# Optimization experiments

Hardware: AMD Instinct MI355X
Metric: run time of the kernel (lower is better)

## Reference

```python
import jax, jax.numpy as jnp
import numpy as np

NUM_AA = 21  # amino-acid alphabet size


def setup_inputs() -> dict:
    key = jax.random.key(0)
    k_x, k_q, k_k, k_v = jax.random.split(key, 4)
    B, L, H, D = 64, 512, 32, 128
    x = jax.random.randint(k_x, (B, L), 0, NUM_AA, dtype=jnp.int32)
    Q = jax.random.normal(k_q, (H, L, D), dtype=jnp.float32)
    K = jax.random.normal(k_k, (H, L, D), dtype=jnp.float32)
    V = jax.random.normal(k_v, (H, NUM_AA, NUM_AA), dtype=jnp.float32)
    return {"x": x, "Q": Q, "K": K, "V": V}


def reference(x, Q, K, V):
    # x: [B, L] int indices in [0, 21); Q,K: [H, L, d_k]; V: [H, q, q]
    d_k = Q.shape[-1]
    L = Q.shape[1]
    # attention over positions, per head: [H, L, L]
    scores = jnp.einsum('hid,hjd->hij', Q, K) / d_k
    A = jax.nn.softmax(scores, axis=-1)
    # coupling tensor J[i, j, a, b] = sum_h A[h, i, j] * V[h, a, b]  -> [L, L, q, q]
    J = jnp.einsum('hij,hab->ijab', A, V)
    # energy[b] = -sum_{i,j} J[i, j, x[b,i], x[b,j]]
    ii = jnp.arange(L)[:, None]        # [L, 1]
    jj = jnp.arange(L)[None, :]        # [1, L]
    vals = J[ii, jj, x[:, :, None], x[:, None, :]]  # broadcast gather -> [B, L, L]
    energy = -jnp.sum(vals, axis=(1, 2))            # [B]
    return energy
```

## Files before the change

### kernel.cpp

```cpp
#include <hip/hip_runtime.h>
#include <hip/hip_bf16.h>
#include <stdint.h>

#define NH  32
#define NL  512
#define ND  128
#define NB  64
#define NAA 21

#define EW_OFF 0
#define QB_OFF (16u << 20)
#define KB_OFF (18u << 20)
#define ZG_OFF (20u << 20)

typedef short bf16x8 __attribute__((ext_vector_type(8)));
typedef float f32x4  __attribute__((ext_vector_type(4)));

static __device__ __forceinline__ uint32_t bf16rtn(float f) {
    uint32_t u = __float_as_uint(f);
    return (u + 0x7fffu + ((u >> 16) & 1u)) >> 16;
}
static __device__ __forceinline__ void gl16(const void* g, void* l) {
    __builtin_amdgcn_global_load_lds(
        (const __attribute__((address_space(1))) uint32_t*)g,
        (__attribute__((address_space(3))) uint32_t*)l, 16, 0, 0);
}

__global__ void prep_qk(const float* __restrict__ Q, const float* __restrict__ K,
                        uint32_t* __restrict__ Qb, uint32_t* __restrict__ Kb) {
    uint32_t tid = blockIdx.x * 256 + threadIdx.x;
    const float* src = (tid >> 20) ? K : Q;
    uint32_t*    dst = (tid >> 20) ? Kb : Qb;
    uint32_t p = tid & 0xFFFFFu;
    uint32_t kk2 = p & 31, r = (p >> 5) & 63, dc = (p >> 11) & 1;
    uint32_t pt = (p >> 12) & 7, h = p >> 15;
    uint32_t pos = pt * 64 + r, d0 = dc * 64 + kk2 * 2;
    float2 v = *(const float2*)(src + ((size_t)(h * NL + pos) * ND + d0));
    uint32_t val = bf16rtn(v.x) | (bf16rtn(v.y) << 16);
    uint32_t byte = (r * 128 + kk2 * 4) ^ ((r & 7) << 4);
    dst[((((h * 8 + pt) * 2 + dc)) << 11) + (byte >> 2)] = val;
}

#define SC_QS 0
#define SC_KS 16384
#define SC_ZS 49152
#define SC_TOT 49408

__global__ __launch_bounds__(512)
void scores_mfma(const uint8_t* __restrict__ Qb, const uint8_t* __restrict__ Kb,
                 uint8_t* __restrict__ Ewsw, float* __restrict__ Zg) {
    extern __shared__ uint8_t smem[];
    int h = blockIdx.x >> 3, it = blockIdx.x & 7;
    int t = threadIdx.x, lane = t & 63, wv = t >> 6;
    int wm = wv >> 1, wn = wv & 1;

    const uint8_t* qsrc = Qb + (((size_t)(h * 8 + it) * 2) << 13);
    gl16(qsrc + t * 16,        smem + SC_QS + t * 16);
    gl16(qsrc + 8192 + t * 16, smem + SC_QS + 8192 + t * 16);
    if (t < 64) *(float*)(smem + SC_ZS + t * 4) = 0.f;

    float zp[2] = {0.f, 0.f};
    for (int sc = 0; sc < 4; ++sc) {
        __syncthreads();
        const uint8_t* ksrc = Kb + (((size_t)(h * 8 + sc * 2) * 2) << 13);
#pragma unroll
        for (int q = 0; q < 4; ++q)
            gl16(ksrc + q * 8192 + t * 16, smem + SC_KS + q * 8192 + t * 16);
        __syncthreads();

        f32x4 acc[2][2];
#pragma unroll
        for (int fm = 0; fm < 2; ++fm)
#pragma unroll
            for (int fn = 0; fn < 2; ++fn) acc[fm][fn] = (f32x4){0.f,0.f,0.f,0.f};

#pragma unroll
        for (int ks = 0; ks < 4; ++ks) {
            int kb = ((ks & 1) * 32 + (lane >> 4) * 8) * 2;
            int dc = ks >> 1;
            bf16x8 af[2], bfr[2];
#pragma unroll
            for (int fm = 0; fm < 2; ++fm) {
                int rr = wm * 32 + fm * 16 + (lane & 15);
                int rt = rr >> 6, r6 = rr & 63;
                af[fm] = *(bf16x8*)(smem + SC_KS + (rt * 2 + dc) * 8192 +
                          (((uint32_t)(r6 * 128 + kb)) ^ ((r6 & 7) << 4)));
            }
#pragma unroll
            for (int fn = 0; fn < 2; ++fn) {
                int rr = wn * 32 + fn * 16 + (lane & 15);
                bfr[fn] = *(bf16x8*)(smem + SC_QS + dc * 8192 +
                          (((uint32_t)(rr * 128 + kb)) ^ ((rr & 7) << 4)));
            }
#pragma unroll
            for (int fm = 0; fm < 2; ++fm)
#pragma unroll
                for (int fn = 0; fn < 2; ++fn)
                    acc[fm][fn] = __builtin_amdgcn_mfma_f32_16x16x32_bf16(
                        af[fm], bfr[fn], acc[fm][fn], 0, 0, 0);
        }
#pragma unroll
        for (int fm = 0; fm < 2; ++fm)
#pragma unroll
            for (int fn = 0; fn < 2; ++fn) {
                float e0 = __expf(acc[fm][fn][0] * 0.0078125f);
                float e1 = __expf(acc[fm][fn][1] * 0.0078125f);
                float e2 = __expf(acc[fm][fn][2] * 0.0078125f);
                float e3 = __expf(acc[fm][fn][3] * 0.0078125f);
                zp[fn] += (e0 + e1) + (e2 + e3);
                uint2 pk;
                pk.x = bf16rtn(e0) | (bf16rtn(e1) << 16);
                pk.y = bf16rtn(e2) | (bf16rtn(e3) << 16);
                int j = sc * 128 + wm * 32 + fm * 16 + (lane >> 4) * 4;
                int i = wn * 32 + fn * 16 + (lane & 15);
                int kc = j >> 6, kk = j & 63;
                uint32_t byte = ((uint32_t)(i * 128 + kk * 2)) ^ ((uint32_t)((i & 7) << 4));
                *(uint2*)(Ewsw + (((size_t)((h * 8 + it) * 8 + kc)) << 13) + byte) = pk;
            }
    }
    zp[0] += __shfl_xor(zp[0], 16); zp[0] += __shfl_xor(zp[0], 32);
    zp[1] += __shfl_xor(zp[1], 16); zp[1] += __shfl_xor(zp[1], 32);
    if (lane < 16) {
        atomicAdd((float*)(smem + SC_ZS) + wn * 32 + lane,      zp[0]);
        atomicAdd((float*)(smem + SC_ZS) + wn * 32 + 16 + lane, zp[1]);
    }
    __syncthreads();
    if (t < 64) Zg[(size_t)h * NL + it * 64 + t] = *((float*)(smem + SC_ZS) + t);
}

#define GE_AB   0
#define GE_RACC 0
#define GE_XS   32768
#define GE_VS   38016
#define GE_TOT  39808

__global__ __launch_bounds__(512, 4)
void gemm_energy(const uint8_t* __restrict__ Ew, const int* __restrict__ x,
                 const float* __restrict__ Zg, const float* __restrict__ V,
                 float* __restrict__ out) {
    extern __shared__ uint8_t smem[];
    uint32_t* xs = (uint32_t*)(smem + GE_XS);
    float*    Vs = (float*)(smem + GE_VS);
    float*    Racc = (float*)(smem + GE_RACC);

    int bid = blockIdx.x;
    int xcd = bid & 7, q = bid >> 3;
    int nb = q % 7, g = (q / 7) * 8 + xcd;
    int h = g >> 2, it = g & 3;
    int n0 = nb * 192;
    int bstart = n0 / 21;
    int bend = (n0 + 191) / 21;
    int bcnt = bend - bstart + 1;

    int t = threadIdx.x, lane = t & 63, wv = t >> 6;
    int wm = wv >> 2, wn = wv & 3;

    const uint8_t* A0 = Ew + (((size_t)(h * 8 + it * 2) * 8) << 13);
    const uint8_t* A1 = Ew + (((size_t)(h * 8 + it * 2 + 1) * 8) << 13);
#define GE_STAGE(p, kc) do { \
        gl16(A0 + (((size_t)(kc)) << 13) + t * 16, smem + GE_AB + (p) * 16384 + t * 16); \
        gl16(A1 + (((size_t)(kc)) << 13) + t * 16, smem + GE_AB + (p) * 16384 + 8192 + t * 16); \
    } while (0)
    GE_STAGE(0, 0);

    for (int idx = t; idx < bcnt * 128; idx += 512) {
        int s = idx >> 7, w = idx & 127;
        int4 xv = *(const int4*)(x + (size_t)(bstart + s) * NL + w * 4);
        xs[s * 129 + w] = (uint32_t)(xv.x & 0xff) | ((uint32_t)(xv.y & 0xff) << 8)
                        | ((uint32_t)(xv.z & 0xff) << 16) | ((uint32_t)(xv.w & 0xff) << 24);
    }
    for (int idx = t; idx < NAA * NAA; idx += 512) Vs[idx] = V[h * (NAA * NAA) + idx];

    int ccol[3], slotc[3];
#pragma unroll
    for (int fn = 0; fn < 3; ++fn) {
        int n = n0 + wn * 48 + fn * 16 + (lane & 15);
        int b = n / 21;
        ccol[fn] = n - b * 21;
        slotc[fn] = b - bstart;
    }

    f32x4 acc[4][3];
#pragma unroll
    for (int fm = 0; fm < 4; ++fm)
#pragma unroll
        for (int fn = 0; fn < 3; ++fn) acc[fm][fn] = (f32x4){0.f,0.f,0.f,0.f};

    __syncthreads();

    for (int kc = 0; kc < 8; ++kc) {
        int p = kc & 1;
        if (kc < 7) GE_STAGE(p ^ 1, kc + 1);
#pragma unroll
        for (int ks = 0; ks < 2; ++ks) {
            int kb = (ks * 32 + (lane >> 4) * 8) * 2;
            bf16x8 af[4];
#pragma unroll
            for (int fm = 0; fm < 4; ++fm) {
                int r6 = fm * 16 + (lane & 15);
                af[fm] = *(bf16x8*)(smem + GE_AB + p * 16384 + wm * 8192 +
                          (((uint32_t)(r6 * 128 + kb)) ^ ((r6 & 7) << 4)));
            }
            int k0w = kc * 16 + ks * 8 + (lane >> 4) * 2;
            bf16x8 bfr[3];
#pragma unroll
            for (int fn = 0; fn < 3; ++fn) {
                uint32_t w0 = xs[slotc[fn] * 129 + k0w];
                uint32_t w1 = xs[slotc[fn] * 129 + k0w + 1];
                uint32_t c = (uint32_t)ccol[fn];
                union { uint32_t u[4]; bf16x8 v; } pk;
#pragma unroll
                for (int pq = 0; pq < 4; ++pq) {
                    uint32_t w = (pq < 2) ? w0 : w1;
                    uint32_t sh = (pq & 1) * 16;
                    uint32_t b0 = (w >> sh) & 0xffu, b1 = (w >> (sh + 8)) & 0xffu;
                    pk.u[pq] = ((b0 == c) ? 0x3F80u : 0u) | ((b1 == c) ? 0x3F800000u : 0u);
                }
                bfr[fn] = pk.v;
            }
#pragma unroll
            for (int fm = 0; fm < 4; ++fm)
#pragma unroll
                for (int fn = 0; fn < 3; ++fn)
                    acc[fm][fn] = __builtin_amdgcn_mfma_f32_16x16x32_bf16(
                        af[fm], bfr[fn], acc[fm][fn], 0, 0, 0);
        }
        __syncthreads();
    }

    float vsum = 0.f;
    int srow = lane & 31;
    int s = wv * 2 + (lane >> 5);
#pragma unroll
    for (int w = 0; w < 4; ++w) {
        if (wm == (w >> 1)) {
#pragma unroll
            for (int f = 0; f < 2; ++f) {
                int fm = (w & 1) * 2 + f;
#pragma unroll
                for (int fn = 0; fn < 3; ++fn) {
                    int col = wn * 48 + fn * 16 + (lane & 15);
                    int rb = f * 16 + (lane >> 4) * 4;
#pragma unroll
                    for (int r = 0; r < 4; ++r)
                        Racc[(rb + r) * 193 + col] = acc[fm][fn][r];
                }
            }
        }
        __syncthreads();
        int ig = it * 128 + w * 32 + srow;
        float rz = 1.0f / Zg[(size_t)h * NL + ig];
        if (s < bcnt) {
            int b = bstart + s;
            uint32_t xw = xs[s * 129 + (ig >> 2)];
            int a = (int)((xw >> ((ig & 3) * 8)) & 0xffu);
            int off = b * 21 - n0;
            int clo = off < 0 ? -off : 0;
            int chi = (192 - off) < 21 ? (192 - off) : 21;
            float dot = 0.f;
            for (int c = clo; c < chi; ++c)
                dot += Vs[a * NAA + c] * Racc[srow * 193 + off + c];
            vsum += dot * rz;
        }
        __syncthreads();
    }
#pragma unroll
    for (int o = 1; o < 32; o <<= 1) vsum += __shfl_xor(vsum, o);
    if (srow == 0 && s < bcnt) atomicAdd(&out[bstart + s], -vsum);
}

extern "C" void kernel_launch(void* const* d_in, const int* in_sizes, int n_in,
                              void* d_out, int out_size, void* d_ws, size_t ws_size,
                              hipStream_t stream) {
    const int*   x = (const int*)d_in[0];
    const float* Q = (const float*)d_in[1];
    const float* K = (const float*)d_in[2];
    const float* V = (const float*)d_in[3];
    float* out = (float*)d_out;
    uint8_t* ws = (uint8_t*)d_ws;

    uint8_t*  Ewsw = ws + EW_OFF;
    uint32_t* Qb   = (uint32_t*)(ws + QB_OFF);
    uint32_t* Kb   = (uint32_t*)(ws + KB_OFF);
    float*    Zg   = (float*)(ws + ZG_OFF);

    hipMemsetAsync(d_out, 0, NB * sizeof(float), stream);
    prep_qk<<<8192, 256, 0, stream>>>(Q, K, Qb, Kb);
    (void)hipFuncSetAttribute((const void*)scores_mfma,
                              hipFuncAttributeMaxDynamicSharedMemorySize, SC_TOT);
    scores_mfma<<<256, 512, SC_TOT, stream>>>((const uint8_t*)Qb, (const uint8_t*)Kb,
                                              Ewsw, Zg);
    (void)hipFuncSetAttribute((const void*)gemm_energy,
                              hipFuncAttributeMaxDynamicSharedMemorySize, GE_TOT);
    gemm_energy<<<896, 512, GE_TOT, stream>>>((const uint8_t*)Ewsw, x, Zg, V, out);
}
```

Before: 79.34 us.

## Precompute one-hot B fragments in a separate kernel and load them from global

Adds a prep kernel that builds the bf16 one-hot B-operand MFMA fragments from x once and writes them to workspace in fragment order. The energy GEMM then loads those fragments from global/L2 instead of rebuilding them per block from LDS with compares and shifts. It also hoists the swizzled A-fragment LDS offsets out of the loop. The trade is an extra kernel launch plus global traffic for B fragments, which are reread by many blocks, in exchange for less ALU and LDS work in the inner loop.

```diff
diff --git a/kernel.cpp b/kernel.cpp
--- a/kernel.cpp
+++ b/kernel.cpp
@@ -12,6 +12,7 @@
 #define QB_OFF (16u << 20)
 #define KB_OFF (18u << 20)
 #define ZG_OFF (20u << 20)
+#define BF_OFF (21u << 20)
 
 typedef short bf16x8 __attribute__((ext_vector_type(8)));
 typedef float f32x4  __attribute__((ext_vector_type(4)));
@@ -39,6 +40,30 @@
     uint32_t val = bf16rtn(v.x) | (bf16rtn(v.y) << 16);
     uint32_t byte = (r * 128 + kk2 * 4) ^ ((r & 7) << 4);
     dst[((((h * 8 + pt) * 2 + dc)) << 11) + (byte >> 2)] = val;
+}
+
+__global__ void prep_bfrag(const int* __restrict__ x, uint8_t* __restrict__ Bf) {
+    int tid = blockIdx.x * 256 + threadIdx.x;
+    int lane = tid & 63;
+    int f  = tid >> 6;
+    int cg = f % 12;
+    int t2 = f / 12;
+    int ks = t2 & 1;
+    int t3 = t2 >> 1;
+    int kc = t3 & 7;
+    int nb = t3 >> 3;
+    int col = nb * 192 + cg * 16 + (lane & 15);
+    int b = col / 21, c = col - b * 21;
+    int k0 = kc * 64 + ks * 32 + (lane >> 4) * 8;
+    const int* xp = x + (size_t)b * NL + k0;
+    int4 x0 = *(const int4*)(xp);
+    int4 x1 = *(const int4*)(xp + 4);
+    uint4 pk;
+    pk.x = ((x0.x == c) ? 0x3F80u : 0u) | ((x0.y == c) ? 0x3F800000u : 0u);
+    pk.y = ((x0.z == c) ? 0x3F80u : 0u) | ((x0.w == c) ? 0x3F800000u : 0u);
+    pk.z = ((x1.x == c) ? 0x3F80u : 0u) | ((x1.y == c) ? 0x3F800000u : 0u);
+    pk.w = ((x1.z == c) ? 0x3F80u : 0u) | ((x1.w == c) ? 0x3F800000u : 0u);
+    *(uint4*)(Bf + (size_t)tid * 16) = pk;
 }
 
 #define SC_QS 0
@@ -135,9 +160,9 @@
 #define GE_TOT  39808
 
 __global__ __launch_bounds__(512, 4)
-void gemm_energy(const uint8_t* __restrict__ Ew, const int* __restrict__ x,
-                 const float* __restrict__ Zg, const float* __restrict__ V,
-                 float* __restrict__ out) {
+void gemm_energy(const uint8_t* __restrict__ Ew, const uint8_t* __restrict__ Bf,
+                 const int* __restrict__ x, const float* __restrict__ Zg,
+                 const float* __restrict__ V, float* __restrict__ out) {
     extern __shared__ uint8_t smem[];
     uint32_t* xs = (uint32_t*)(smem + GE_XS);
     float*    Vs = (float*)(smem + GE_VS);
@@ -171,14 +196,18 @@
     }
     for (int idx = t; idx < NAA * NAA; idx += 512) Vs[idx] = V[h * (NAA * NAA) + idx];
 
-    int ccol[3], slotc[3];
-#pragma unroll
-    for (int fn = 0; fn < 3; ++fn) {
-        int n = n0 + wn * 48 + fn * 16 + (lane & 15);
-        int b = n / 21;
-        ccol[fn] = n - b * 21;
-        slotc[fn] = b - bstart;
-    }
+    const uint8_t* bfw = Bf + ((size_t)(nb * 192 + 3 * wn)) * 1024 + lane * 16;
+
+    uint32_t aoff[2][4];
+#pragma unroll
+    for (int ks = 0; ks < 2; ++ks)
+#pragma unroll
+        for (int fm = 0; fm < 4; ++fm) {
+            int r6 = fm * 16 + (lane & 15);
+            int kb = (ks * 32 + (lane >> 4) * 8) * 2;
+            aoff[ks][fm] = (uint32_t)(wm * 8192 +
+                           (((uint32_t)(r6 * 128 + kb)) ^ ((r6 & 7) << 4)));
+        }
 
     f32x4 acc[4][3];
 #pragma unroll
@@ -191,39 +220,24 @@
     for (int kc = 0; kc < 8; ++kc) {
         int p = kc & 1;
         if (kc < 7) GE_STAGE(p ^ 1, kc + 1);
+        bf16x8 bfr[2][3];
+#pragma unroll
+        for (int ks = 0; ks < 2; ++ks)
+#pragma unroll
+            for (int fn = 0; fn < 3; ++fn)
+                bfr[ks][fn] = *(const bf16x8*)(bfw + kc * 24576 + ks * 12288 + fn * 1024);
 #pragma unroll
         for (int ks = 0; ks < 2; ++ks) {
-            int kb = (ks * 32 + (lane >> 4) * 8) * 2;
             bf16x8 af[4];
 #pragma unroll
-            for (int fm = 0; fm < 4; ++fm) {
-                int r6 = fm * 16 + (lane & 15);
-                af[fm] = *(bf16x8*)(smem + GE_AB + p * 16384 + wm * 8192 +
-                          (((uint32_t)(r6 * 128 + kb)) ^ ((r6 & 7) << 4)));
-            }
-            int k0w = kc * 16 + ks * 8 + (lane >> 4) * 2;
-            bf16x8 bfr[3];
-#pragma unroll
-            for (int fn = 0; fn < 3; ++fn) {
-                uint32_t w0 = xs[slotc[fn] * 129 + k0w];
-                uint32_t w1 = xs[slotc[fn] * 129 + k0w + 1];
-                uint32_t c = (uint32_t)ccol[fn];
-                union { uint32_t u[4]; bf16x8 v; } pk;
-#pragma unroll
-                for (int pq = 0; pq < 4; ++pq) {
-                    uint32_t w = (pq < 2) ? w0 : w1;
-                    uint32_t sh = (pq & 1) * 16;
-                    uint32_t b0 = (w >> sh) & 0xffu, b1 = (w >> (sh + 8)) & 0xffu;
-                    pk.u[pq] = ((b0 == c) ? 0x3F80u : 0u) | ((b1 == c) ? 0x3F800000u : 0u);
-                }
-                bfr[fn] = pk.v;
-            }
+            for (int fm = 0; fm < 4; ++fm)
+                af[fm] = *(bf16x8*)(smem + GE_AB + p * 16384 + aoff[ks][fm]);
 #pragma unroll
             for (int fm = 0; fm < 4; ++fm)
 #pragma unroll
                 for (int fn = 0; fn < 3; ++fn)
                     acc[fm][fn] = __builtin_amdgcn_mfma_f32_16x16x32_bf16(
-                        af[fm], bfr[fn], acc[fm][fn], 0, 0, 0);
+                        af[fm], bfr[ks][fn], acc[fm][fn], 0, 0, 0);
         }
         __syncthreads();
     }
@@ -283,14 +297,16 @@
     uint32_t* Qb   = (uint32_t*)(ws + QB_OFF);
     uint32_t* Kb   = (uint32_t*)(ws + KB_OFF);
     float*    Zg   = (float*)(ws + ZG_OFF);
+    uint8_t*  Bfr  = ws + BF_OFF;
 
     hipMemsetAsync(d_out, 0, NB * sizeof(float), stream);
     prep_qk<<<8192, 256, 0, stream>>>(Q, K, Qb, Kb);
+    prep_bfrag<<<336, 256, 0, stream>>>(x, Bfr);
     (void)hipFuncSetAttribute((const void*)scores_mfma,
                               hipFuncAttributeMaxDynamicSharedMemorySize, SC_TOT);
     scores_mfma<<<256, 512, SC_TOT, stream>>>((const uint8_t*)Qb, (const uint8_t*)Kb,
                                               Ewsw, Zg);
     (void)hipFuncSetAttribute((const void*)gemm_energy,
                               hipFuncAttributeMaxDynamicSharedMemorySize, GE_TOT);
-    gemm_energy<<<896, 512, GE_TOT, stream>>>((const uint8_t*)Ewsw, x, Zg, V, out);
-}
+    gemm_energy<<<896, 512, GE_TOT, stream>>>((const uint8_t*)Ewsw, Bfr, x, Zg, V, out);
+}
```

After: 78.73 us. About the same (-0.8%).

## Fuse scores and energy GEMM into one kernel keeping exp-scores in LDS

Applied to the files above, without the earlier changes.

Merges the scores kernel and the energy GEMM kernel into a single kernel. Each block computes its 64-row tile of exponentiated scores into LDS, then runs the one-hot GEMM over all 64 batches (21 accumulator fragments per wave) and the V contraction directly from LDS. This removes the global round trip of the score matrix and the row-sum array, plus one launch. In exchange the kernel uses about 150KB of LDS with only 256 blocks, and the wide accumulator array raises register pressure and lowers occupancy.

```diff
diff --git a/kernel.cpp b/kernel.cpp
--- a/kernel.cpp
+++ b/kernel.cpp
@@ -8,10 +8,8 @@
 #define NB  64
 #define NAA 21
 
-#define EW_OFF 0
 #define QB_OFF (16u << 20)
 #define KB_OFF (18u << 20)
-#define ZG_OFF (20u << 20)
 
 typedef short bf16x8 __attribute__((ext_vector_type(8)));
 typedef float f32x4  __attribute__((ext_vector_type(4)));
@@ -41,232 +39,182 @@
     dst[((((h * 8 + pt) * 2 + dc)) << 11) + (byte >> 2)] = val;
 }
 
-#define SC_QS 0
-#define SC_KS 16384
-#define SC_ZS 49152
-#define SC_TOT 49408
-
-__global__ __launch_bounds__(512)
-void scores_mfma(const uint8_t* __restrict__ Qb, const uint8_t* __restrict__ Kb,
-                 uint8_t* __restrict__ Ewsw, float* __restrict__ Zg) {
+#define FA_A   0
+#define FA_STG 65536
+#define FA_XS  114688
+#define FA_VS  147968
+#define FA_ZS  149760
+#define FA_TOT 150016
+
+__global__ __launch_bounds__(512, 2)
+void fused_energy(const uint8_t* __restrict__ Qb, const uint8_t* __restrict__ Kb,
+                  const int* __restrict__ x, const float* __restrict__ V,
+                  float* __restrict__ out) {
     extern __shared__ uint8_t smem[];
+    uint8_t*  Al  = smem + FA_A;
+    uint32_t* xs  = (uint32_t*)(smem + FA_XS);
+    float*    Vs  = (float*)(smem + FA_VS);
+    float*    Zl  = (float*)(smem + FA_ZS);
+    float*    Racc = (float*)(smem + FA_STG);
+
     int h = blockIdx.x >> 3, it = blockIdx.x & 7;
     int t = threadIdx.x, lane = t & 63, wv = t >> 6;
-    int wm = wv >> 1, wn = wv & 1;
 
     const uint8_t* qsrc = Qb + (((size_t)(h * 8 + it) * 2) << 13);
-    gl16(qsrc + t * 16,        smem + SC_QS + t * 16);
-    gl16(qsrc + 8192 + t * 16, smem + SC_QS + 8192 + t * 16);
-    if (t < 64) *(float*)(smem + SC_ZS + t * 4) = 0.f;
-
-    float zp[2] = {0.f, 0.f};
-    for (int sc = 0; sc < 4; ++sc) {
+    gl16(qsrc + t * 16,        smem + FA_STG + t * 16);
+    gl16(qsrc + 8192 + t * 16, smem + FA_STG + 8192 + t * 16);
+    for (int idx = t; idx < 64 * 128; idx += 512) {
+        int s = idx >> 7, w = idx & 127;
+        int4 xv = *(const int4*)(x + (size_t)s * NL + w * 4);
+        xs[s * 130 + w] = (uint32_t)(xv.x & 0xff) | ((uint32_t)(xv.y & 0xff) << 8)
+                        | ((uint32_t)(xv.z & 0xff) << 16) | ((uint32_t)(xv.w & 0xff) << 24);
+    }
+    for (int idx = t; idx < NAA * NAA; idx += 512) Vs[idx] = V[h * (NAA * NAA) + idx];
+    if (t < 64) Zl[t] = 0.f;
+
+    {
+        int wm = wv >> 1, wn = wv & 1;
+        float zp[2] = {0.f, 0.f};
+        for (int sc = 0; sc < 4; ++sc) {
+            __syncthreads();
+            const uint8_t* ksrc = Kb + (((size_t)(h * 8 + sc * 2) * 2) << 13);
+#pragma unroll
+            for (int q = 0; q < 4; ++q)
+                gl16(ksrc + q * 8192 + t * 16, smem + FA_STG + 16384 + q * 8192 + t * 16);
+            __syncthreads();
+
+            f32x4 acc[2][2];
+#pragma unroll
+            for (int fm = 0; fm < 2; ++fm)
+#pragma unroll
+                for (int fn = 0; fn < 2; ++fn) acc[fm][fn] = (f32x4){0.f,0.f,0.f,0.f};
+#pragma unroll
+            for (int ks = 0; ks < 4; ++ks) {
+                int kb = ((ks & 1) * 32 + (lane >> 4) * 8) * 2;
+                int dc = ks >> 1;
+                bf16x8 af[2], bfr[2];
+#pragma unroll
+                for (int fm = 0; fm < 2; ++fm) {
+                    int rr = wm * 32 + fm * 16 + (lane & 15);
+                    int rt = rr >> 6, r6 = rr & 63;
+                    af[fm] = *(bf16x8*)(smem + FA_STG + 16384 + (rt * 2 + dc) * 8192 +
+                              (((uint32_t)(r6 * 128 + kb)) ^ ((r6 & 7) << 4)));
+                }
+#pragma unroll
+                for (int fn = 0; fn < 2; ++fn) {
+                    int rr = wn * 32 + fn * 16 + (lane & 15);
+                    bfr[fn] = *(bf16x8*)(smem + FA_STG + dc * 8192 +
+                              (((uint32_t)(rr * 128 + kb)) ^ ((rr & 7) << 4)));
+                }
+#pragma unroll
+                for (int fm = 0; fm < 2; ++fm)
+#pragma unroll
+                    for (int fn = 0; fn < 2; ++fn)
+                        acc[fm][fn] = __builtin_amdgcn_mfma_f32_16x16x32_bf16(
+                            af[fm], bfr[fn], acc[fm][fn], 0, 0, 0);
+            }
+#pragma unroll
+            for (int fm = 0; fm < 2; ++fm)
+#pragma unroll
+                for (int fn = 0; fn < 2; ++fn) {
+                    float e0 = __expf(acc[fm][fn][0] * 0.0078125f);
+                    float e1 = __expf(acc[fm][fn][1] * 0.0078125f);
+                    float e2 = __expf(acc[fm][fn][2] * 0.0078125f);
+                    float e3 = __expf(acc[fm][fn][3] * 0.0078125f);
+                    zp[fn] += (e0 + e1) + (e2 + e3);
+                    uint2 pk;
+                    pk.x = bf16rtn(e0) | (bf16rtn(e1) << 16);
+                    pk.y = bf16rtn(e2) | (bf16rtn(e3) << 16);
+                    int j = sc * 128 + wm * 32 + fm * 16 + (lane >> 4) * 4;
+                    int i = wn * 32 + fn * 16 + (lane & 15);
+                    int kc = j >> 6, kk = j & 63;
+                    uint32_t byte = ((uint32_t)(i * 128 + kk * 2)) ^ ((uint32_t)((i & 7) << 4));
+                    *(uint2*)(Al + (kc << 13) + byte) = pk;
+                }
+        }
+        zp[0] += __shfl_xor(zp[0], 16); zp[0] += __shfl_xor(zp[0], 32);
+        zp[1] += __shfl_xor(zp[1], 16); zp[1] += __shfl_xor(zp[1], 32);
+        if (lane < 16) {
+            atomicAdd(&Zl[wn * 32 + lane],      zp[0]);
+            atomicAdd(&Zl[wn * 32 + 16 + lane], zp[1]);
+        }
+    }
+    __syncthreads();
+
+    int wm = wv >> 2, wn = wv & 3;
+    int pc[NAA];
+#pragma unroll
+    for (int fn = 0; fn < NAA; ++fn) {
+        int n = wn * 336 + fn * 16 + (lane & 15);
+        int b = n / 21;
+        pc[fn] = (b << 8) | (n - b * 21);
+    }
+
+    f32x4 acc[2][NAA];
+#pragma unroll
+    for (int fm = 0; fm < 2; ++fm)
+#pragma unroll
+        for (int fn = 0; fn < NAA; ++fn) acc[fm][fn] = (f32x4){0.f,0.f,0.f,0.f};
+
+    for (int q = 0; q < 16; ++q) {
+        int kb = ((q & 1) * 32 + (lane >> 4) * 8) * 2;
+        bf16x8 af[2];
+#pragma unroll
+        for (int fm = 0; fm < 2; ++fm) {
+            int r6 = wm * 32 + fm * 16 + (lane & 15);
+            af[fm] = *(bf16x8*)(Al + ((q >> 1) << 13) +
+                      (((uint32_t)(r6 * 128 + kb)) ^ ((r6 & 7) << 4)));
+        }
+        int k0w = q * 8 + (lane >> 4) * 2;
+#pragma unroll
+        for (int fn = 0; fn < NAA; ++fn) {
+            int b = pc[fn] >> 8;
+            uint32_t c = (uint32_t)(pc[fn] & 0xff);
+            uint2 ww = *(const uint2*)(xs + b * 130 + k0w);
+            union { uint32_t u[4]; bf16x8 v; } pk;
+#pragma unroll
+            for (int pq = 0; pq < 4; ++pq) {
+                uint32_t w = (pq < 2) ? ww.x : ww.y;
+                uint32_t sh = (pq & 1) * 16;
+                uint32_t b0 = (w >> sh) & 0xffu, b1 = (w >> (sh + 8)) & 0xffu;
+                pk.u[pq] = ((b0 == c) ? 0x3F80u : 0u) | ((b1 == c) ? 0x3F800000u : 0u);
+            }
+            acc[0][fn] = __builtin_amdgcn_mfma_f32_16x16x32_bf16(af[0], pk.v, acc[0][fn], 0, 0, 0);
+            acc[1][fn] = __builtin_amdgcn_mfma_f32_16x16x32_bf16(af[1], pk.v, acc[1][fn], 0, 0, 0);
+        }
+    }
+
+    float vsum = 0.f;
+    int bt = wv * 8 + (lane >> 3);
+    int row = lane & 7;
+#pragma unroll
+    for (int w = 0; w < 8; ++w) {
         __syncthreads();
-        const uint8_t* ksrc = Kb + (((size_t)(h * 8 + sc * 2) * 2) << 13);
-#pragma unroll
-        for (int q = 0; q < 4; ++q)
-            gl16(ksrc + q * 8192 + t * 16, smem + SC_KS + q * 8192 + t * 16);
+        if (wm == (w >> 2) && ((lane >> 4) >> 1) == (w & 1)) {
+            int fm = (w >> 1) & 1;
+            int lrb = ((lane >> 4) & 1) * 4;
+#pragma unroll
+            for (int fn = 0; fn < NAA; ++fn)
+#pragma unroll
+                for (int r = 0; r < 4; ++r)
+                    Racc[(lrb + r) * 1349 + wn * 336 + fn * 16 + (lane & 15)] =
+                        acc[fm][fn][r];
+        }
         __syncthreads();
-
-        f32x4 acc[2][2];
-#pragma unroll
-        for (int fm = 0; fm < 2; ++fm)
-#pragma unroll
-            for (int fn = 0; fn < 2; ++fn) acc[fm][fn] = (f32x4){0.f,0.f,0.f,0.f};
-
-#pragma unroll
-        for (int ks = 0; ks < 4; ++ks) {
-            int kb = ((ks & 1) * 32 + (lane >> 4) * 8) * 2;
-            int dc = ks >> 1;
-            bf16x8 af[2], bfr[2];
-#pragma unroll
-            for (int fm = 0; fm < 2; ++fm) {
-                int rr = wm * 32 + fm * 16 + (lane & 15);
-                int rt = rr >> 6, r6 = rr & 63;
-                af[fm] = *(bf16x8*)(smem + SC_KS + (rt * 2 + dc) * 8192 +
-                          (((uint32_t)(r6 * 128 + kb)) ^ ((r6 & 7) << 4)));
-            }
-#pragma unroll
-            for (int fn = 0; fn < 2; ++fn) {
-                int rr = wn * 32 + fn * 16 + (lane & 15);
-                bfr[fn] = *(bf16x8*)(smem + SC_QS + dc * 8192 +
-                          (((uint32_t)(rr * 128 + kb)) ^ ((rr & 7) << 4)));
-            }
-#pragma unroll
-            for (int fm = 0; fm < 2; ++fm)
-#pragma unroll
-                for (int fn = 0; fn < 2; ++fn)
-                    acc[fm][fn] = __builtin_amdgcn_mfma_f32_16x16x32_bf16(
-                        af[fm], bfr[fn], acc[fm][fn], 0, 0, 0);
-        }
-#pragma unroll
-        for (int fm = 0; fm < 2; ++fm)
-#pragma unroll
-            for (int fn = 0; fn < 2; ++fn) {
-                float e0 = __expf(acc[fm][fn][0] * 0.0078125f);
-                float e1 = __expf(acc[fm][fn][1] * 0.0078125f);
-                float e2 = __expf(acc[fm][fn][2] * 0.0078125f);
-                float e3 = __expf(acc[fm][fn][3] * 0.0078125f);
-                zp[fn] += (e0 + e1) + (e2 + e3);
-                uint2 pk;
-                pk.x = bf16rtn(e0) | (bf16rtn(e1) << 16);
-                pk.y = bf16rtn(e2) | (bf16rtn(e3) << 16);
-                int j = sc * 128 + wm * 32 + fm * 16 + (lane >> 4) * 4;
-                int i = wn * 32 + fn * 16 + (lane & 15);
-                int kc = j >> 6, kk = j & 63;
-                uint32_t byte = ((uint32_t)(i * 128 + kk * 2)) ^ ((uint32_t)((i & 7) << 4));
-                *(uint2*)(Ewsw + (((size_t)((h * 8 + it) * 8 + kc)) << 13) + byte) = pk;
-            }
-    }
-    zp[0] += __shfl_xor(zp[0], 16); zp[0] += __shfl_xor(zp[0], 32);
-    zp[1] += __shfl_xor(zp[1], 16); zp[1] += __shfl_xor(zp[1], 32);
-    if (lane < 16) {
-        atomicAdd((float*)(smem + SC_ZS) + wn * 32 + lane,      zp[0]);
-        atomicAdd((float*)(smem + SC_ZS) + wn * 32 + 16 + lane, zp[1]);
-    }
-    __syncthreads();
-    if (t < 64) Zg[(size_t)h * NL + it * 64 + t] = *((float*)(smem + SC_ZS) + t);
-}
-
-#define GE_AB   0
-#define GE_RACC 0
-#define GE_XS   32768
-#define GE_VS   38016
-#define GE_TOT  39808
-
-__global__ __launch_bounds__(512, 4)
-void gemm_energy(const uint8_t* __restrict__ Ew, const int* __restrict__ x,
-                 const float* __restrict__ Zg, const float* __restrict__ V,
-                 float* __restrict__ out) {
-    extern __shared__ uint8_t smem[];
-    uint32_t* xs = (uint32_t*)(smem + GE_XS);
-    float*    Vs = (float*)(smem + GE_VS);
-    float*    Racc = (float*)(smem + GE_RACC);
-
-    int bid = blockIdx.x;
-    int xcd = bid & 7, q = bid >> 3;
-    int nb = q % 7, g = (q / 7) * 8 + xcd;
-    int h = g >> 2, it = g & 3;
-    int n0 = nb * 192;
-    int bstart = n0 / 21;
-    int bend = (n0 + 191) / 21;
-    int bcnt = bend - bstart + 1;
-
-    int t = threadIdx.x, lane = t & 63, wv = t >> 6;
-    int wm = wv >> 2, wn = wv & 3;
-
-    const uint8_t* A0 = Ew + (((size_t)(h * 8 + it * 2) * 8) << 13);
-    const uint8_t* A1 = Ew + (((size_t)(h * 8 + it * 2 + 1) * 8) << 13);
-#define GE_STAGE(p, kc) do { \
-        gl16(A0 + (((size_t)(kc)) << 13) + t * 16, smem + GE_AB + (p) * 16384 + t * 16); \
-        gl16(A1 + (((size_t)(kc)) << 13) + t * 16, smem + GE_AB + (p) * 16384 + 8192 + t * 16); \
-    } while (0)
-    GE_STAGE(0, 0);
-
-    for (int idx = t; idx < bcnt * 128; idx += 512) {
-        int s = idx >> 7, w = idx & 127;
-        int4 xv = *(const int4*)(x + (size_t)(bstart + s) * NL + w * 4);
-        xs[s * 129 + w] = (uint32_t)(xv.x & 0xff) | ((uint32_t)(xv.y & 0xff) << 8)
-                        | ((uint32_t)(xv.z & 0xff) << 16) | ((uint32_t)(xv.w & 0xff) << 24);
-    }
-    for (int idx = t; idx < NAA * NAA; idx += 512) Vs[idx] = V[h * (NAA * NAA) + idx];
-
-    int ccol[3], slotc[3];
-#pragma unroll
-    for (int fn = 0; fn < 3; ++fn) {
-        int n = n0 + wn * 48 + fn * 16 + (lane & 15);
-        int b = n / 21;
-        ccol[fn] = n - b * 21;
-        slotc[fn] = b - bstart;
-    }
-
-    f32x4 acc[4][3];
-#pragma unroll
-    for (int fm = 0; fm < 4; ++fm)
-#pragma unroll
-        for (int fn = 0; fn < 3; ++fn) acc[fm][fn] = (f32x4){0.f,0.f,0.f,0.f};
-
-    __syncthreads();
-
-    for (int kc = 0; kc < 8; ++kc) {
-        int p = kc & 1;
-        if (kc < 7) GE_STAGE(p ^ 1, kc + 1);
-#pragma unroll
-        for (int ks = 0; ks < 2; ++ks) {
-            int kb = (ks * 32 + (lane >> 4) * 8) * 2;
-            bf16x8 af[4];
-#pragma unroll
-            for (int fm = 0; fm < 4; ++fm) {
-                int r6 = fm * 16 + (lane & 15);
-                af[fm] = *(bf16x8*)(smem + GE_AB + p * 16384 + wm * 8192 +
-                          (((uint32_t)(r6 * 128 + kb)) ^ ((r6 & 7) << 4)));
-            }
-            int k0w = kc * 16 + ks * 8 + (lane >> 4) * 2;
-            bf16x8 bfr[3];
-#pragma unroll
-            for (int fn = 0; fn < 3; ++fn) {
-                uint32_t w0 = xs[slotc[fn] * 129 + k0w];
-                uint32_t w1 = xs[slotc[fn] * 129 + k0w + 1];
-                uint32_t c = (uint32_t)ccol[fn];
-                union { uint32_t u[4]; bf16x8 v; } pk;
-#pragma unroll
-                for (int pq = 0; pq < 4; ++pq) {
-                    uint32_t w = (pq < 2) ? w0 : w1;
-                    uint32_t sh = (pq & 1) * 16;
-                    uint32_t b0 = (w >> sh) & 0xffu, b1 = (w >> (sh + 8)) & 0xffu;
-                    pk.u[pq] = ((b0 == c) ? 0x3F80u : 0u) | ((b1 == c) ? 0x3F800000u : 0u);
-                }
-                bfr[fn] = pk.v;
-            }
-#pragma unroll
-            for (int fm = 0; fm < 4; ++fm)
-#pragma unroll
-                for (int fn = 0; fn < 3; ++fn)
-                    acc[fm][fn] = __builtin_amdgcn_mfma_f32_16x16x32_bf16(
-                        af[fm], bfr[fn], acc[fm][fn], 0, 0, 0);
-        }
-        __syncthreads();
-    }
-
-    float vsum = 0.f;
-    int srow = lane & 31;
-    int s = wv * 2 + (lane >> 5);
-#pragma unroll
-    for (int w = 0; w < 4; ++w) {
-        if (wm == (w >> 1)) {
-#pragma unroll
-            for (int f = 0; f < 2; ++f) {
-                int fm = (w & 1) * 2 + f;
-#pragma unroll
-                for (int fn = 0; fn < 3; ++fn) {
-                    int col = wn * 48 + fn * 16 + (lane & 15);
-                    int rb = f * 16 + (lane >> 4) * 4;
-#pragma unroll
-                    for (int r = 0; r < 4; ++r)
-                        Racc[(rb + r) * 193 + col] = acc[fm][fn][r];
-                }
-            }
-        }
-        __syncthreads();
-        int ig = it * 128 + w * 32 + srow;
-        float rz = 1.0f / Zg[(size_t)h * NL + ig];
-        if (s < bcnt) {
-            int b = bstart + s;
-            uint32_t xw = xs[s * 129 + (ig >> 2)];
-            int a = (int)((xw >> ((ig & 3) * 8)) & 0xffu);
-            int off = b * 21 - n0;
-            int clo = off < 0 ? -off : 0;
-            int chi = (192 - off) < 21 ? (192 - off) : 21;
-            float dot = 0.f;
-            for (int c = clo; c < chi; ++c)
-                dot += Vs[a * NAA + c] * Racc[srow * 193 + off + c];
-            vsum += dot * rz;
-        }
-        __syncthreads();
-    }
-#pragma unroll
-    for (int o = 1; o < 32; o <<= 1) vsum += __shfl_xor(vsum, o);
-    if (srow == 0 && s < bcnt) atomicAdd(&out[bstart + s], -vsum);
+        int ig = it * 64 + w * 8 + row;
+        uint32_t xw = xs[bt * 130 + (ig >> 2)];
+        int a = (int)((xw >> ((ig & 3) * 8)) & 0xffu);
+        float rz = 1.0f / Zl[w * 8 + row];
+        float dot = 0.f;
+#pragma unroll
+        for (int c = 0; c < NAA; ++c)
+            dot += Vs[a * NAA + c] * Racc[row * 1349 + bt * 21 + c];
+        vsum += dot * rz;
+    }
+    vsum += __shfl_xor(vsum, 1);
+    vsum += __shfl_xor(vsum, 2);
+    vsum += __shfl_xor(vsum, 4);
+    if (row == 0) atomicAdd(&out[bt], -vsum);
 }
 
 extern "C" void kernel_launch(void* const* d_in, const int* in_sizes, int n_in,
@@ -279,18 +227,13 @@
     float* out = (float*)d_out;
     uint8_t* ws = (uint8_t*)d_ws;
 
-    uint8_t*  Ewsw = ws + EW_OFF;
-    uint32_t* Qb   = (uint32_t*)(ws + QB_OFF);
-    uint32_t* Kb   = (uint32_t*)(ws + KB_OFF);
-    float*    Zg   = (float*)(ws + ZG_OFF);
+    uint32_t* Qb = (uint32_t*)(ws + QB_OFF);
+    uint32_t* Kb = (uint32_t*)(ws + KB_OFF);
 
     hipMemsetAsync(d_out, 0, NB * sizeof(float), stream);
     prep_qk<<<8192, 256, 0, stream>>>(Q, K, Qb, Kb);
-    (void)hipFuncSetAttribute((const void*)scores_mfma,
-                              hipFuncAttributeMaxDynamicSharedMemorySize, SC_TOT);
-    scores_mfma<<<256, 512, SC_TOT, stream>>>((const uint8_t*)Qb, (const uint8_t*)Kb,
-                                              Ewsw, Zg);
-    (void)hipFuncSetAttribute((const void*)gemm_energy,
-                              hipFuncAttributeMaxDynamicSharedMemorySize, GE_TOT);
-    gemm_energy<<<896, 512, GE_TOT, stream>>>((const uint8_t*)Ewsw, x, Zg, V, out);
-}
+    (void)hipFuncSetAttribute((const void*)fused_energy,
+                              hipFuncAttributeMaxDynamicSharedMemorySize, FA_TOT);
+    fused_energy<<<256, 512, FA_TOT, stream>>>((const uint8_t*)Qb, (const uint8_t*)Kb,
+                                               x, V, out);
+}
```

Measured after the change: 100.9 us. +27.1%, slower.
